# Kernel optimization log

Measured on AMD Instinct MI355X. Metric: run time of the kernel, lower is better.

Reference implementation:

```python
import jax, jax.numpy as jnp
import numpy as np

WINDOW = 7
HEADS = 4
HEAD_DIM = 32
DISP = WINDOW // 2  # shifted displacement = 3
SCALE = HEADS ** (-0.5)  # faithful to source (heads, not head_dim)


def _create_mask(ws, d, upper_lower, left_right):
    m = np.zeros((ws * ws, ws * ws), dtype=np.float32)
    if upper_lower:
        m[-d * ws:, :-d * ws] = -np.inf
        m[:-d * ws, -d * ws:] = -np.inf
    if left_right:
        m = m.reshape(ws, ws, ws, ws)
        m[:, -d:, :, :-d] = -np.inf
        m[:, :-d, :, -d:] = -np.inf
        m = m.reshape(ws * ws, ws * ws)
    return m


def _relative_indices(ws):
    coords = np.array([[x, y] for x in range(ws) for y in range(ws)])
    return (coords[None, :, :] - coords[:, None, :]) + ws - 1  # (ws^2, ws^2, 2)


def setup_inputs() -> dict:
    key = jax.random.key(0)
    k1, k2, k3, k4 = jax.random.split(key, 4)
    inner = HEADS * HEAD_DIM
    return {
        "x": jax.random.normal(k1, (64, 56, 56, 128), dtype=jnp.float32),
        "w_qkv": jax.random.normal(k2, (3 * inner, 128), dtype=jnp.float32) * 0.02,
        "pos_embedding": jax.random.normal(k3, (2 * WINDOW - 1, 2 * WINDOW - 1), dtype=jnp.float32),
        "w_out": jax.random.normal(k4, (128, inner), dtype=jnp.float32) * 0.02,
        "b_out": jnp.zeros((128,), dtype=jnp.float32),
    }


def _to_windows(t, ws, heads, hd):
    b, H, W, _ = t.shape
    nwh, nww = H // ws, W // ws
    t = t.reshape(b, nwh, ws, nww, ws, heads, hd)
    # -> (b, h, nw, ws^2, d)
    return t.transpose(0, 5, 1, 3, 2, 4, 6).reshape(b, heads, nwh * nww, ws * ws, hd)


def _from_windows(t, ws, nwh, nww):
    b, h, nw, s2, d = t.shape
    t = t.reshape(b, h, nwh, nww, ws, ws, d)
    # -> (b, H, W, h*d)
    return t.transpose(0, 2, 4, 3, 5, 1, 6).reshape(b, nwh * ws, nww * ws, h * d)


def reference(x, w_qkv, pos_embedding, w_out, b_out):
    ws = WINDOW
    b, H, W, _ = x.shape
    nwh, nww = H // ws, W // ws

    # cyclic shift
    x = jnp.roll(x, shift=(-DISP, -DISP), axis=(1, 2))

    qkv = x @ w_qkv.T  # (b,H,W,3*inner)
    q, k, v = jnp.split(qkv, 3, axis=-1)
    q = _to_windows(q, ws, HEADS, HEAD_DIM)
    k = _to_windows(k, ws, HEADS, HEAD_DIM)
    v = _to_windows(v, ws, HEADS, HEAD_DIM)

    scores = jnp.einsum('bhwid,bhwjd->bhwij', q, k) * SCALE

    # relative position bias gather
    ri = _relative_indices(ws)
    bias = pos_embedding[ri[:, :, 0], ri[:, :, 1]]  # (ws^2, ws^2)
    scores = scores + bias

    # shift masks added only to specific window rows/columns
    ul = _create_mask(ws, DISP, True, False)
    lr = _create_mask(ws, DISP, False, True)
    full_mask = np.zeros((nwh * nww, ws * ws, ws * ws), dtype=np.float32)
    full_mask[-nww:] += ul
    full_mask[nww - 1::nww] += lr
    scores = scores + jnp.asarray(full_mask)

    probs = jax.nn.softmax(scores, axis=-1)
    attn = jnp.einsum('bhwij,bhwjd->bhwid', probs, v)

    out = _from_windows(attn, ws, nwh, nww)
    out = out @ w_out.T + b_out
    out = jnp.roll(out, shift=(DISP, DISP), axis=(1, 2))
    return out
```

## Files before the change

### kernel.cpp

```cpp
#include <hip/hip_runtime.h>

#define IMG 56
#define CH  128
#define S2  49
#define DSP 3
#define MTS 50

#define LDA   128
#define LDQK  256
#define LDP   64
#define LDVT  64
#define OFF_QK 12544
#define OFF_VT 37632
#define SMEM_BYTES 54016

typedef __attribute__((ext_vector_type(8))) short bf16x8;
typedef __attribute__((ext_vector_type(4))) float f32x4;

__device__ __forceinline__ unsigned short f2bs(float f) {
    unsigned u = __float_as_uint(f);
    return (unsigned short)((u + 0x7fffu + ((u >> 16) & 1u)) >> 16);
}

__device__ __forceinline__ int idxA(int row, int col) {
    return row * LDA + ((((col >> 3) ^ row) & 7) << 3) + ((col >> 3) & ~7) * 8 + (col & 7);
}
__device__ __forceinline__ int idxA2(int row, int col) {
    int blk = (col >> 3) ^ (row & 7);
    return row * LDA + blk * 8 + (col & 7);
}
__device__ __forceinline__ int idxQK(int row, int col) {
    int blk = (col >> 3) ^ (row & 7);
    return row * LDQK + blk * 8 + (col & 7);
}

__global__ __launch_bounds__(256)
void swin_prep(const float* __restrict__ w_qkv,
               const float* __restrict__ w_out,
               const float* __restrict__ pe,
               unsigned short* __restrict__ wqb,
               unsigned short* __restrict__ wob,
               float* __restrict__ mt4)
{
    const int tid = (int)(blockIdx.x * blockDim.x + threadIdx.x);
    const int np  = (int)(gridDim.x * blockDim.x);
    for (int i = tid; i < 384 * CH; i += np) wqb[i] = f2bs(w_qkv[i]);
    for (int i = tid; i < CH * CH;  i += np) wob[i] = f2bs(w_out[i]);
    for (int i = tid; i < 4 * S2 * S2; i += np) {
        const int v  = i / (S2 * S2), r = i - v * (S2 * S2);
        const int ii = r / S2, jj = r - ii * S2;
        const int iy = ii / 7, ix = ii - iy * 7;
        const int jy = jj / 7, jx = jj - jy * 7;
        float val = pe[(jy - iy + 6) * 13 + (jx - ix + 6)];
        if ((v & 2) && ((iy >= 4) != (jy >= 4))) val = -1e30f;
        if ((v & 1) && ((ix >= 4) != (jx >= 4))) val = -1e30f;
        mt4[v * (S2 * MTS) + ii * MTS + jj] = val;
    }
}

__global__ __launch_bounds__(256, 3)
void swin_fused(const float* __restrict__ x,
                const unsigned short* __restrict__ wqb,
                const float* __restrict__ mt4,
                const unsigned short* __restrict__ wob,
                const float* __restrict__ b_out,
                float* __restrict__ out)
{
    __shared__ __align__(16) char smem[SMEM_BYTES];
    unsigned short* const ldsA  = (unsigned short*)smem;
    unsigned short* const ldsQK = (unsigned short*)(smem + OFF_QK);
    unsigned short* const ldsVT = (unsigned short*)(smem + OFF_VT);

    const int tid  = (int)threadIdx.x;
    const int wave = tid >> 6, lane = tid & 63;
    const int lm   = lane & 15, lq = lane >> 4;
    const int b    = (int)blockIdx.y;
    const int wh   = (int)blockIdx.x >> 3, ww = (int)blockIdx.x & 7;
    const bool my  = (wh == 7), mx = (ww == 7);
    const float* const mtg = mt4 + (((my ? 2 : 0) + (mx ? 1 : 0)) * (S2 * MTS));

    {
        unsigned long long* vz = (unsigned long long*)(smem + OFF_VT);
        for (int i = tid; i < 2048; i += 256) vz[i] = 0ull;
    }
    for (int idx = tid; idx < S2 * 32; idx += 256) {
        const int s  = idx >> 5, c4 = (idx & 31) << 2;
        const int iy = s / 7, ix = s - iy * 7;
        int gy = wh * 7 + iy + DSP; if (gy >= IMG) gy -= IMG;
        int gx = ww * 7 + ix + DSP; if (gx >= IMG) gx -= IMG;
        const float4 v = *(const float4*)(x + (size_t)((b * IMG + gy) * IMG + gx) * CH + c4);
        uint2 p;
        p.x = (unsigned)f2bs(v.x) | ((unsigned)f2bs(v.y) << 16);
        p.y = (unsigned)f2bs(v.z) | ((unsigned)f2bs(v.w) << 16);
        *(uint2*)(ldsA + idxA2(s, c4)) = p;
    }
    __syncthreads();

    {
        bf16x8 af[4][4];
        #pragma unroll
        for (int mt = 0; mt < 4; ++mt)
            #pragma unroll
            for (int kt = 0; kt < 4; ++kt)
                af[mt][kt] = *(const bf16x8*)(ldsA + idxA2(mt * 16 + lm, kt * 32 + lq * 8));

        #pragma unroll
        for (int nt = 0; nt < 6; ++nt) {
            const int n0 = (wave * 6 + nt) * 16;
            const unsigned short* wb = wqb + (size_t)(n0 + lm) * CH + lq * 8;
            bf16x8 bf[4];
            #pragma unroll
            for (int kt = 0; kt < 4; ++kt)
                bf[kt] = *(const bf16x8*)(wb + kt * 32);
            f32x4 c0 = {0.f,0.f,0.f,0.f}, c1 = {0.f,0.f,0.f,0.f};
            f32x4 c2 = {0.f,0.f,0.f,0.f}, c3 = {0.f,0.f,0.f,0.f};
            #pragma unroll
            for (int kt = 0; kt < 4; ++kt) {
                c0 = __builtin_amdgcn_mfma_f32_16x16x32_bf16(af[0][kt], bf[kt], c0, 0, 0, 0);
                c1 = __builtin_amdgcn_mfma_f32_16x16x32_bf16(af[1][kt], bf[kt], c1, 0, 0, 0);
                c2 = __builtin_amdgcn_mfma_f32_16x16x32_bf16(af[2][kt], bf[kt], c2, 0, 0, 0);
                c3 = __builtin_amdgcn_mfma_f32_16x16x32_bf16(af[3][kt], bf[kt], c3, 0, 0, 0);
            }
            const int col = n0 + lm;
            #pragma unroll
            for (int mt = 0; mt < 4; ++mt) {
                const f32x4 c = (mt == 0) ? c0 : (mt == 1) ? c1 : (mt == 2) ? c2 : c3;
                const int rb = mt * 16 + lq * 4;
                #pragma unroll
                for (int r = 0; r < 4; ++r) {
                    const int row = rb + r;
                    if (row < S2) {
                        const unsigned short hv = f2bs(c[r]);
                        if (col < 256) {
                            ldsQK[idxQK(row, col)] = hv;
                        } else {
                            const int d   = col - 256;
                            const int blk = (row >> 3) ^ (d & 7);
                            ldsVT[d * LDVT + blk * 8 + (row & 7)] = hv;
                        }
                    }
                }
            }
        }
    }
    __syncthreads();

    {
        const int h = wave;
        unsigned short* const ldsP = (unsigned short*)(smem + OFF_QK + wave * 6272);

        bf16x8 qa[4], kb[4];
        #pragma unroll
        for (int mt = 0; mt < 4; ++mt)
            qa[mt] = *(const bf16x8*)(ldsQK + idxQK(mt * 16 + lm, h * 32 + lq * 8));
        #pragma unroll
        for (int nt = 0; nt < 4; ++nt)
            kb[nt] = *(const bf16x8*)(ldsQK + idxQK(nt * 16 + lm, CH + h * 32 + lq * 8));

        f32x4 c[4][4];
        #pragma unroll
        for (int mt = 0; mt < 4; ++mt)
            #pragma unroll
            for (int nt = 0; nt < 4; ++nt) {
                f32x4 z = {0.f, 0.f, 0.f, 0.f};
                c[mt][nt] = __builtin_amdgcn_mfma_f32_16x16x32_bf16(qa[mt], kb[nt], z, 0, 0, 0);
            }

        __syncthreads();

        bool colok[4];
        #pragma unroll
        for (int nt = 0; nt < 4; ++nt) colok[nt] = (nt * 16 + lm) < S2;

        #pragma unroll
        for (int mt = 0; mt < 4; ++mt) {
            #pragma unroll
            for (int r = 0; r < 4; ++r) {
                const int row  = mt * 16 + lq * 4 + r;
                const int rowc = row < S2 ? row : (S2 - 1);
                const float* mrow = mtg + rowc * MTS + lm;
                #pragma unroll
                for (int nt = 0; nt < 4; ++nt) {
                    const float v = c[mt][nt][r] * 0.5f + mrow[nt * 16];
                    c[mt][nt][r] = colok[nt] ? v : -1e30f;
                }
                float mm = fmaxf(fmaxf(c[mt][0][r], c[mt][1][r]), fmaxf(c[mt][2][r], c[mt][3][r]));
                mm = fmaxf(mm, __shfl_xor(mm, 1));
                mm = fmaxf(mm, __shfl_xor(mm, 2));
                mm = fmaxf(mm, __shfl_xor(mm, 4));
                mm = fmaxf(mm, __shfl_xor(mm, 8));
                const float p0 = __expf(c[mt][0][r] - mm);
                const float p1 = __expf(c[mt][1][r] - mm);
                const float p2 = __expf(c[mt][2][r] - mm);
                const float p3 = __expf(c[mt][3][r] - mm);
                float ll = (p0 + p1) + (p2 + p3);
                ll += __shfl_xor(ll, 1);
                ll += __shfl_xor(ll, 2);
                ll += __shfl_xor(ll, 4);
                ll += __shfl_xor(ll, 8);
                const float inv = 1.0f / ll;
                c[mt][0][r] = p0 * inv; c[mt][1][r] = p1 * inv;
                c[mt][2][r] = p2 * inv; c[mt][3][r] = p3 * inv;
            }
        }

        #pragma unroll
        for (int mt = 0; mt < 4; ++mt)
            #pragma unroll
            for (int r = 0; r < 4; ++r) {
                const int row = mt * 16 + lq * 4 + r;
                if (row < S2) {
                    #pragma unroll
                    for (int nt = 0; nt < 4; ++nt) {
                        const int col = nt * 16 + lm;
                        const int blk = (col >> 3) ^ (row & 7);
                        ldsP[row * LDP + blk * 8 + (col & 7)] = f2bs(c[mt][nt][r]);
                    }
                }
            }

        bf16x8 pa[4][2], vb[2][2];
        #pragma unroll
        for (int mt = 0; mt < 4; ++mt) {
            const int row = mt * 16 + lm;
            #pragma unroll
            for (int kt = 0; kt < 2; ++kt) {
                const int blk = (kt * 4 + lq) ^ (row & 7);
                pa[mt][kt] = *(const bf16x8*)(ldsP + row * LDP + blk * 8);
            }
        }
        #pragma unroll
        for (int nt = 0; nt < 2; ++nt) {
            const int d = h * 32 + nt * 16 + lm;
            #pragma unroll
            for (int kt = 0; kt < 2; ++kt) {
                const int blk = (kt * 4 + lq) ^ (d & 7);
                vb[nt][kt] = *(const bf16x8*)(ldsVT + d * LDVT + blk * 8);
            }
        }
        f32x4 oc[4][2];
        #pragma unroll
        for (int mt = 0; mt < 4; ++mt)
            #pragma unroll
            for (int nt = 0; nt < 2; ++nt) {
                f32x4 z = {0.f, 0.f, 0.f, 0.f};
                z = __builtin_amdgcn_mfma_f32_16x16x32_bf16(pa[mt][0], vb[nt][0], z, 0, 0, 0);
                oc[mt][nt] = __builtin_amdgcn_mfma_f32_16x16x32_bf16(pa[mt][1], vb[nt][1], z, 0, 0, 0);
            }

        #pragma unroll
        for (int mt = 0; mt < 4; ++mt)
            #pragma unroll
            for (int r = 0; r < 4; ++r) {
                const int row = mt * 16 + lq * 4 + r;
                if (row < S2) {
                    #pragma unroll
                    for (int nt = 0; nt < 2; ++nt)
                        ldsA[idxA2(row, h * 32 + nt * 16 + lm)] = f2bs(oc[mt][nt][r]);
                }
            }
    }
    __syncthreads();

    {
        bf16x8 af[4][4];
        #pragma unroll
        for (int mt = 0; mt < 4; ++mt)
            #pragma unroll
            for (int kt = 0; kt < 4; ++kt)
                af[mt][kt] = *(const bf16x8*)(ldsA + idxA2(mt * 16 + lm, kt * 32 + lq * 8));

        #pragma unroll
        for (int nt = 0; nt < 2; ++nt) {
            const int n0 = (wave * 2 + nt) * 16;
            const unsigned short* wb = wob + (size_t)(n0 + lm) * CH + lq * 8;
            bf16x8 bf[4];
            #pragma unroll
            for (int kt = 0; kt < 4; ++kt)
                bf[kt] = *(const bf16x8*)(wb + kt * 32);
            f32x4 c0 = {0.f,0.f,0.f,0.f}, c1 = {0.f,0.f,0.f,0.f};
            f32x4 c2 = {0.f,0.f,0.f,0.f}, c3 = {0.f,0.f,0.f,0.f};
            #pragma unroll
            for (int kt = 0; kt < 4; ++kt) {
                c0 = __builtin_amdgcn_mfma_f32_16x16x32_bf16(af[0][kt], bf[kt], c0, 0, 0, 0);
                c1 = __builtin_amdgcn_mfma_f32_16x16x32_bf16(af[1][kt], bf[kt], c1, 0, 0, 0);
                c2 = __builtin_amdgcn_mfma_f32_16x16x32_bf16(af[2][kt], bf[kt], c2, 0, 0, 0);
                c3 = __builtin_amdgcn_mfma_f32_16x16x32_bf16(af[3][kt], bf[kt], c3, 0, 0, 0);
            }
            const int col = n0 + lm;
            const float bo = b_out[col];
            #pragma unroll
            for (int mt = 0; mt < 4; ++mt) {
                const f32x4 c = (mt == 0) ? c0 : (mt == 1) ? c1 : (mt == 2) ? c2 : c3;
                const int rb = mt * 16 + lq * 4;
                #pragma unroll
                for (int r = 0; r < 4; ++r) {
                    const int s = rb + r;
                    if (s < S2) {
                        const int sy = s / 7, sx = s - sy * 7;
                        int gy = wh * 7 + sy + DSP; if (gy >= IMG) gy -= IMG;
                        int gx = ww * 7 + sx + DSP; if (gx >= IMG) gx -= IMG;
                        out[(size_t)((b * IMG + gy) * IMG + gx) * CH + col] = c[r] + bo;
                    }
                }
            }
        }
    }
}

extern "C" void kernel_launch(void* const* d_in, const int* in_sizes, int n_in,
                              void* d_out, int out_size, void* d_ws, size_t ws_size,
                              hipStream_t stream) {
    const float* x      = (const float*)d_in[0];
    const float* w_qkv  = (const float*)d_in[1];
    const float* pe     = (const float*)d_in[2];
    const float* w_out  = (const float*)d_in[3];
    const float* b_out  = (const float*)d_in[4];
    float* out = (float*)d_out;

    unsigned short* wqb = (unsigned short*)d_ws;
    unsigned short* wob = (unsigned short*)((char*)d_ws + 98304);
    float*          mt4 = (float*)((char*)d_ws + 131072);

    swin_prep<<<dim3(128), 256, 0, stream>>>(w_qkv, w_out, pe, wqb, wob, mt4);

    dim3 grid(64, 64);
    swin_fused<<<grid, 256, 0, stream>>>(x, wqb, mt4, wob, b_out, out);
}
```

Measured before the change: 304.5 us.

## Alias LDS buffers to cut shared memory and raise occupancy to four blocks

Shares one LDS region between the input tile, the V-transpose buffer and the attention output, and shrinks the V row stride, cutting the LDS footprint so four blocks can fit per CU (launch bounds raised from 3 to 4). Extra barriers are added so the aliased regions are not overwritten while still being read. V is now stored with packed 64-bit writes in place of per-element swizzled stores. Softmax drops the max-subtraction and exponentiates the biased scores directly, which saves shuffles but risks overflow if scores get large; padded rows are clamped to row 48 instead of reading beyond the valid rows.

```diff
diff --git a/kernel.cpp b/kernel.cpp
--- a/kernel.cpp
+++ b/kernel.cpp
@@ -5,14 +5,14 @@
 #define S2  49
 #define DSP 3
 #define MTS 50
+#define MVS 2500
 
 #define LDA   128
 #define LDQK  256
 #define LDP   64
-#define LDVT  64
-#define OFF_QK 12544
-#define OFF_VT 37632
-#define SMEM_BYTES 54016
+#define LDVT  56
+#define OFF_U 25088
+#define SMEM_BYTES 39440
 
 typedef __attribute__((ext_vector_type(8))) short bf16x8;
 typedef __attribute__((ext_vector_type(4))) float f32x4;
@@ -22,9 +22,6 @@
     return (unsigned short)((u + 0x7fffu + ((u >> 16) & 1u)) >> 16);
 }
 
-__device__ __forceinline__ int idxA(int row, int col) {
-    return row * LDA + ((((col >> 3) ^ row) & 7) << 3) + ((col >> 3) & ~7) * 8 + (col & 7);
-}
 __device__ __forceinline__ int idxA2(int row, int col) {
     int blk = (col >> 3) ^ (row & 7);
     return row * LDA + blk * 8 + (col & 7);
@@ -54,11 +51,11 @@
         float val = pe[(jy - iy + 6) * 13 + (jx - ix + 6)];
         if ((v & 2) && ((iy >= 4) != (jy >= 4))) val = -1e30f;
         if ((v & 1) && ((ix >= 4) != (jx >= 4))) val = -1e30f;
-        mt4[v * (S2 * MTS) + ii * MTS + jj] = val;
-    }
-}
-
-__global__ __launch_bounds__(256, 3)
+        mt4[v * MVS + ii * MTS + jj] = val;
+    }
+}
+
+__global__ __launch_bounds__(256, 4)
 void swin_fused(const float* __restrict__ x,
                 const unsigned short* __restrict__ wqb,
                 const float* __restrict__ mt4,
@@ -67,9 +64,8 @@
                 float* __restrict__ out)
 {
     __shared__ __align__(16) char smem[SMEM_BYTES];
-    unsigned short* const ldsA  = (unsigned short*)smem;
-    unsigned short* const ldsQK = (unsigned short*)(smem + OFF_QK);
-    unsigned short* const ldsVT = (unsigned short*)(smem + OFF_VT);
+    unsigned short* const ldsQK = (unsigned short*)smem;
+    unsigned short* const ldsU  = (unsigned short*)(smem + OFF_U);
 
     const int tid  = (int)threadIdx.x;
     const int wave = tid >> 6, lane = tid & 63;
@@ -77,12 +73,9 @@
     const int b    = (int)blockIdx.y;
     const int wh   = (int)blockIdx.x >> 3, ww = (int)blockIdx.x & 7;
     const bool my  = (wh == 7), mx = (ww == 7);
-    const float* const mtg = mt4 + (((my ? 2 : 0) + (mx ? 1 : 0)) * (S2 * MTS));
-
-    {
-        unsigned long long* vz = (unsigned long long*)(smem + OFF_VT);
-        for (int i = tid; i < 2048; i += 256) vz[i] = 0ull;
-    }
+    const float* const mtg = mt4 + (((my ? 2 : 0) + (mx ? 1 : 0)) * MVS);
+
+    if (tid < 2) ((unsigned long long*)(smem + OFF_U + 2 * (size_t)CH * LDVT))[tid] = 0ull;
     for (int idx = tid; idx < S2 * 32; idx += 256) {
         const int s  = idx >> 5, c4 = (idx & 31) << 2;
         const int iy = s / 7, ix = s - iy * 7;
@@ -92,17 +85,20 @@
         uint2 p;
         p.x = (unsigned)f2bs(v.x) | ((unsigned)f2bs(v.y) << 16);
         p.y = (unsigned)f2bs(v.z) | ((unsigned)f2bs(v.w) << 16);
-        *(uint2*)(ldsA + idxA2(s, c4)) = p;
+        *(uint2*)(ldsU + idxA2(s, c4)) = p;
     }
     __syncthreads();
 
     {
         bf16x8 af[4][4];
         #pragma unroll
-        for (int mt = 0; mt < 4; ++mt)
+        for (int mt = 0; mt < 4; ++mt) {
+            const int row = (mt < 3) ? (mt * 16 + lm) : 48;
             #pragma unroll
             for (int kt = 0; kt < 4; ++kt)
-                af[mt][kt] = *(const bf16x8*)(ldsA + idxA2(mt * 16 + lm, kt * 32 + lq * 8));
+                af[mt][kt] = *(const bf16x8*)(ldsU + idxA2(row, kt * 32 + lq * 8));
+        }
+        __syncthreads();
 
         #pragma unroll
         for (int nt = 0; nt < 6; ++nt) {
@@ -122,22 +118,31 @@
                 c3 = __builtin_amdgcn_mfma_f32_16x16x32_bf16(af[3][kt], bf[kt], c3, 0, 0, 0);
             }
             const int col = n0 + lm;
-            #pragma unroll
-            for (int mt = 0; mt < 4; ++mt) {
-                const f32x4 c = (mt == 0) ? c0 : (mt == 1) ? c1 : (mt == 2) ? c2 : c3;
-                const int rb = mt * 16 + lq * 4;
+            if (n0 < 256) {
                 #pragma unroll
-                for (int r = 0; r < 4; ++r) {
-                    const int row = rb + r;
-                    if (row < S2) {
-                        const unsigned short hv = f2bs(c[r]);
-                        if (col < 256) {
-                            ldsQK[idxQK(row, col)] = hv;
-                        } else {
-                            const int d   = col - 256;
-                            const int blk = (row >> 3) ^ (d & 7);
-                            ldsVT[d * LDVT + blk * 8 + (row & 7)] = hv;
+                for (int mt = 0; mt < 4; ++mt) {
+                    const f32x4 c = (mt == 0) ? c0 : (mt == 1) ? c1 : (mt == 2) ? c2 : c3;
+                    const int rb = mt * 16 + lq * 4;
+                    #pragma unroll
+                    for (int r = 0; r < 4; ++r) {
+                        const int row = rb + r;
+                        if (row < S2) ldsQK[idxQK(row, col)] = f2bs(c[r]);
+                    }
+                }
+            } else {
+                const int d = col - 256;
+                #pragma unroll
+                for (int mt = 0; mt < 4; ++mt) {
+                    const f32x4 c = (mt == 0) ? c0 : (mt == 1) ? c1 : (mt == 2) ? c2 : c3;
+                    const int rb = mt * 16 + lq * 4;
+                    if (rb < LDVT) {
+                        unsigned long long pk = 0;
+                        #pragma unroll
+                        for (int r = 0; r < 4; ++r) {
+                            const unsigned short us = (rb + r < S2) ? f2bs(c[r]) : (unsigned short)0;
+                            pk |= (unsigned long long)us << (16 * r);
                         }
+                        *(unsigned long long*)(ldsU + (size_t)d * LDVT + rb) = pk;
                     }
                 }
             }
@@ -147,7 +152,7 @@
 
     {
         const int h = wave;
-        unsigned short* const ldsP = (unsigned short*)(smem + OFF_QK + wave * 6272);
+        unsigned short* const ldsP = (unsigned short*)(smem + wave * 6272);
 
         bf16x8 qa[4], kb[4];
         #pragma unroll
@@ -179,20 +184,10 @@
                 const int row  = mt * 16 + lq * 4 + r;
                 const int rowc = row < S2 ? row : (S2 - 1);
                 const float* mrow = mtg + rowc * MTS + lm;
-                #pragma unroll
-                for (int nt = 0; nt < 4; ++nt) {
-                    const float v = c[mt][nt][r] * 0.5f + mrow[nt * 16];
-                    c[mt][nt][r] = colok[nt] ? v : -1e30f;
-                }
-                float mm = fmaxf(fmaxf(c[mt][0][r], c[mt][1][r]), fmaxf(c[mt][2][r], c[mt][3][r]));
-                mm = fmaxf(mm, __shfl_xor(mm, 1));
-                mm = fmaxf(mm, __shfl_xor(mm, 2));
-                mm = fmaxf(mm, __shfl_xor(mm, 4));
-                mm = fmaxf(mm, __shfl_xor(mm, 8));
-                const float p0 = __expf(c[mt][0][r] - mm);
-                const float p1 = __expf(c[mt][1][r] - mm);
-                const float p2 = __expf(c[mt][2][r] - mm);
-                const float p3 = __expf(c[mt][3][r] - mm);
+                const float p0 = colok[0] ? __expf(c[mt][0][r] * 0.5f + mrow[0])  : 0.f;
+                const float p1 = colok[1] ? __expf(c[mt][1][r] * 0.5f + mrow[16]) : 0.f;
+                const float p2 = colok[2] ? __expf(c[mt][2][r] * 0.5f + mrow[32]) : 0.f;
+                const float p3 = colok[3] ? __expf(c[mt][3][r] * 0.5f + mrow[48]) : 0.f;
                 float ll = (p0 + p1) + (p2 + p3);
                 ll += __shfl_xor(ll, 1);
                 ll += __shfl_xor(ll, 2);
@@ -233,11 +228,11 @@
         for (int nt = 0; nt < 2; ++nt) {
             const int d = h * 32 + nt * 16 + lm;
             #pragma unroll
-            for (int kt = 0; kt < 2; ++kt) {
-                const int blk = (kt * 4 + lq) ^ (d & 7);
-                vb[nt][kt] = *(const bf16x8*)(ldsVT + d * LDVT + blk * 8);
-            }
-        }
+            for (int kt = 0; kt < 2; ++kt)
+                vb[nt][kt] = *(const bf16x8*)(ldsU + (size_t)d * LDVT + kt * 32 + lq * 8);
+        }
+        __syncthreads();
+
         f32x4 oc[4][2];
         #pragma unroll
         for (int mt = 0; mt < 4; ++mt)
@@ -256,7 +251,7 @@
                 if (row < S2) {
                     #pragma unroll
                     for (int nt = 0; nt < 2; ++nt)
-                        ldsA[idxA2(row, h * 32 + nt * 16 + lm)] = f2bs(oc[mt][nt][r]);
+                        ldsU[idxA2(row, h * 32 + nt * 16 + lm)] = f2bs(oc[mt][nt][r]);
                 }
             }
     }
@@ -265,10 +260,12 @@
     {
         bf16x8 af[4][4];
         #pragma unroll
-        for (int mt = 0; mt < 4; ++mt)
+        for (int mt = 0; mt < 4; ++mt) {
+            const int row = (mt < 3) ? (mt * 16 + lm) : 48;
             #pragma unroll
             for (int kt = 0; kt < 4; ++kt)
-                af[mt][kt] = *(const bf16x8*)(ldsA + idxA2(mt * 16 + lm, kt * 32 + lq * 8));
+                af[mt][kt] = *(const bf16x8*)(ldsU + idxA2(row, kt * 32 + lq * 8));
+        }
 
         #pragma unroll
         for (int nt = 0; nt < 2; ++nt) {
```

After: 298.6 us. About the same (-1.9%).
